# Optimization experiments

Measured on AMD Instinct MI355X. Metric: run time of the kernel, lower is better.

The kernel has to match this reference:

```python
import jax, jax.numpy as jnp
import numpy as np

S = 8192  # query length
T = 8192  # key/value length
D = 256   # head dim


def setup_inputs() -> dict:
    key = jax.random.key(0)
    kq, kk, kv = jax.random.split(key, 3)
    return {
        "query": jax.random.normal(kq, (S, D), dtype=jnp.float32),
        "key": jax.random.normal(kk, (T, D), dtype=jnp.float32),
        "value": jax.random.normal(kv, (T, D), dtype=jnp.float32),
    }


def reference(query, key, value):
    # attn_weights = Q @ K^T  (contract last dims, no batch dims)  -> [S, T]
    attn_weights = jnp.einsum("sd,td->st", query, key)
    # SoftmaxAttn: softmax over axes [ndim//2, ndim) == last axis for 2D
    attn_weights = jax.nn.softmax(attn_weights, axis=-1).astype(jnp.float32)
    # y = A @ V  -> [S, D]
    y = jnp.einsum("st,td->sd", attn_weights, value)
    return y
```

## Files before the change

### kernel.cpp

```cpp
#include <hip/hip_runtime.h>
#include <hip/hip_fp16.h>

#define S_LEN 8192
#define T_LEN 8192
#define D_DIM 256
#define QBLK 256
#define KVBLK 32
#define TSPLIT 8
#define TCHUNK (T_LEN / TSPLIT)
#define NKV (TCHUNK / KVBLK)
#define NQT (S_LEN / QBLK)
#define KTILE_BYTES 16384
#define VTILE_BYTES 16384
#define RESCALE_THR 4.0f

typedef _Float16 f16x8 __attribute__((ext_vector_type(8)));
typedef float f32x4 __attribute__((ext_vector_type(4)));

struct h4 { _Float16 h[4]; };

#define GLOAD_LDS16(g, l)                                              \
    __builtin_amdgcn_global_load_lds(                                  \
        (const __attribute__((address_space(1))) void*)(g),            \
        (__attribute__((address_space(3))) void*)(l), 16, 0, 0)

#define MFMA16(a, b, c) __builtin_amdgcn_mfma_f32_16x16x32_f16(a, b, c, 0, 0, 0)

__global__ __launch_bounds__(256) void cvt_kernel(const float* __restrict__ in,
                                                  _Float16* __restrict__ out, int n4) {
    int i = blockIdx.x * 256 + threadIdx.x;
    if (i < n4) {
        float4 v = ((const float4*)in)[i];
        h4 o;
        o.h[0] = (_Float16)v.x; o.h[1] = (_Float16)v.y;
        o.h[2] = (_Float16)v.z; o.h[3] = (_Float16)v.w;
        ((h4*)out)[i] = o;
    }
}

__global__ __launch_bounds__(256) void cvt_swz_kernel(const float* __restrict__ in,
                                                      _Float16* __restrict__ img,
                                                      int nchunks) {
    int id = blockIdx.x * 256 + threadIdx.x;
    if (id >= nchunks) return;
    int row = id >> 5, ck = id & 31;
    int t = row >> 5, r = row & 31;
    float4 a = *(const float4*)(in + (size_t)row * D_DIM + ck * 8);
    float4 b = *(const float4*)(in + (size_t)row * D_DIM + ck * 8 + 4);
    f16x8 o;
    o[0] = (_Float16)a.x; o[1] = (_Float16)a.y; o[2] = (_Float16)a.z; o[3] = (_Float16)a.w;
    o[4] = (_Float16)b.x; o[5] = (_Float16)b.y; o[6] = (_Float16)b.z; o[7] = (_Float16)b.w;
    *(f16x8*)((char*)img + (size_t)t * KTILE_BYTES + r * 512 + ((ck ^ (r & 7)) << 4)) = o;
}

__global__ __launch_bounds__(256) void vt_swz_kernel(const float* __restrict__ V,
                                                     _Float16* __restrict__ Vimg) {
    __shared__ float tile[32][260];
    const int t = blockIdx.x;
#pragma unroll
    for (int i = 0; i < 8; ++i) {
        int idx = i * 256 + threadIdx.x;
        int kr = idx >> 6, c4 = idx & 63;
        float4 v = *(const float4*)(V + ((size_t)t * 32 + kr) * D_DIM + c4 * 4);
        tile[kr][c4 * 4 + 0] = v.x;
        tile[kr][c4 * 4 + 1] = v.y;
        tile[kr][c4 * 4 + 2] = v.z;
        tile[kr][c4 * 4 + 3] = v.w;
    }
    __syncthreads();
#pragma unroll
    for (int i = 0; i < 4; ++i) {
        int gid = i * 256 + threadIdx.x;
        int d = gid >> 2, gk = gid & 3;
        f16x8 o;
#pragma unroll
        for (int j = 0; j < 8; ++j) o[j] = (_Float16)tile[gk * 8 + j][d];
        *(f16x8*)((char*)Vimg + (size_t)t * VTILE_BYTES + d * 64 +
                  ((gk ^ (d & 3)) << 4)) = o;
    }
}

__global__ __launch_bounds__(512, 2) void attn_kernel(
    const _Float16* __restrict__ Qh, const _Float16* __restrict__ Kimg,
    const _Float16* __restrict__ Vimg, _Float16* __restrict__ Opart,
    float* __restrict__ ml) {
    __shared__ __align__(16) char smem[65536];
    const int tid = threadIdx.x;
    const int wave = tid >> 6, lane = tid & 63;
    const int g = lane >> 4, c = lane & 15;
    const int qtile = blockIdx.x, split = blockIdx.y;
    const int tile0 = split * NKV;

    f16x8 qf[2][8];
    {
        const size_t qrow0 = (size_t)qtile * QBLK + wave * 32 + c;
#pragma unroll
        for (int mi = 0; mi < 2; ++mi)
#pragma unroll
            for (int ks = 0; ks < 8; ++ks)
                qf[mi][ks] =
                    *(const f16x8*)(Qh + (qrow0 + mi * 16) * D_DIM + (ks * 4 + g) * 8);
    }

    f32x4 acc[2][16];
#pragma unroll
    for (int mi = 0; mi < 2; ++mi)
#pragma unroll
        for (int dt = 0; dt < 16; ++dt) acc[mi][dt] = (f32x4){0.f, 0.f, 0.f, 0.f};
    float m[2] = {-1e30f, -1e30f}, l[2] = {0.f, 0.f};

    const int stg_l = wave * 1024;
    const int stg_g = stg_l + lane * 16;

    {
        const char* Kt = (const char*)Kimg + (size_t)tile0 * KTILE_BYTES;
        const char* Vt = (const char*)Vimg + (size_t)tile0 * VTILE_BYTES;
#pragma unroll
        for (int i = 0; i < 2; ++i) {
            GLOAD_LDS16(Kt + i * 8192 + stg_g, smem + i * 8192 + stg_l);
            GLOAD_LDS16(Vt + i * 8192 + stg_g, smem + 32768 + i * 8192 + stg_l);
        }
    }

    for (int kt = 0; kt < NKV; ++kt) {
        const int cur = kt & 1;
        if (kt + 1 < NKV) {
            const char* Kt = (const char*)Kimg + (size_t)(tile0 + kt + 1) * KTILE_BYTES;
            const char* Vt = (const char*)Vimg + (size_t)(tile0 + kt + 1) * VTILE_BYTES;
            const int nb = (cur ^ 1) * 16384;
#pragma unroll
            for (int i = 0; i < 2; ++i) {
                GLOAD_LDS16(Kt + i * 8192 + stg_g, smem + nb + i * 8192 + stg_l);
                GLOAD_LDS16(Vt + i * 8192 + stg_g, smem + 32768 + nb + i * 8192 + stg_l);
            }
            asm volatile("s_waitcnt vmcnt(4)" ::: "memory");
        } else {
            asm volatile("s_waitcnt vmcnt(0)" ::: "memory");
        }
        __builtin_amdgcn_s_barrier();

        const char* sK = smem + cur * 16384;
        const char* sV = smem + 32768 + cur * 16384;

        f32x4 st[2][2];
#pragma unroll
        for (int mi = 0; mi < 2; ++mi)
#pragma unroll
            for (int ct = 0; ct < 2; ++ct) st[mi][ct] = (f32x4){0.f, 0.f, 0.f, 0.f};
        __builtin_amdgcn_s_setprio(1);
#pragma unroll
        for (int ks = 0; ks < 8; ++ks) {
            const int ck = ((ks * 4 + g) ^ (c & 7)) << 4;
            f16x8 kf0 = *(const f16x8*)(sK + c * 512 + ck);
            f16x8 kf1 = *(const f16x8*)(sK + 8192 + c * 512 + ck);
            st[0][0] = MFMA16(kf0, qf[0][ks], st[0][0]);
            st[0][1] = MFMA16(kf1, qf[0][ks], st[0][1]);
            st[1][0] = MFMA16(kf0, qf[1][ks], st[1][0]);
            st[1][1] = MFMA16(kf1, qf[1][ks], st[1][1]);
        }
        __builtin_amdgcn_s_setprio(0);

        unsigned int pk[2][2][2];
#pragma unroll
        for (int mi = 0; mi < 2; ++mi) {
            float pm = st[mi][0][0];
#pragma unroll
            for (int ct = 0; ct < 2; ++ct)
#pragma unroll
                for (int r = 0; r < 4; ++r) pm = fmaxf(pm, st[mi][ct][r]);
            pm = fmaxf(pm, __shfl_xor(pm, 16));
            pm = fmaxf(pm, __shfl_xor(pm, 32));
            if (__any(pm > m[mi] + RESCALE_THR)) {
                float mn = fmaxf(m[mi], pm);
                float sc = __expf(m[mi] - mn);
                m[mi] = mn;
                l[mi] *= sc;
                float fr[4];
#pragma unroll
                for (int r = 0; r < 4; ++r) fr[r] = __shfl(sc, (g << 4) | (g * 4 + r));
#pragma unroll
                for (int dt = 0; dt < 16; ++dt)
#pragma unroll
                    for (int r = 0; r < 4; ++r) acc[mi][dt][r] *= fr[r];
            }
            float rs = 0.f;
#pragma unroll
            for (int ct = 0; ct < 2; ++ct)
#pragma unroll
                for (int r = 0; r < 4; ++r) {
                    float p = __expf(st[mi][ct][r] - m[mi]);
                    st[mi][ct][r] = p;
                    rs += p;
                }
            rs += __shfl_xor(rs, 16);
            rs += __shfl_xor(rs, 32);
            l[mi] += rs;
#pragma unroll
            for (int ct = 0; ct < 2; ++ct) {
                pk[mi][ct][0] = __builtin_bit_cast(
                    unsigned int,
                    __builtin_amdgcn_cvt_pkrtz(st[mi][ct][0], st[mi][ct][1]));
                pk[mi][ct][1] = __builtin_bit_cast(
                    unsigned int,
                    __builtin_amdgcn_cvt_pkrtz(st[mi][ct][2], st[mi][ct][3]));
            }
        }

        union PU { unsigned int u[4]; f16x8 v; };
        PU pu[2];
#pragma unroll
        for (int mi = 0; mi < 2; ++mi)
#pragma unroll
            for (int w = 0; w < 4; ++w) {
                int src = ((((g & 1) << 1) + (w >> 1)) << 4) | c;
                int t0 = __shfl((int)pk[mi][0][w & 1], src);
                int t1 = __shfl((int)pk[mi][1][w & 1], src);
                pu[mi].u[w] = (unsigned int)((g >> 1) ? t1 : t0);
            }

        __builtin_amdgcn_s_setprio(1);
#pragma unroll
        for (int dt = 0; dt < 16; ++dt) {
            f16x8 vf = *(const f16x8*)(sV + (dt * 16 + c) * 64 + ((g ^ (c & 3)) << 4));
            acc[0][dt] = MFMA16(pu[0].v, vf, acc[0][dt]);
            acc[1][dt] = MFMA16(pu[1].v, vf, acc[1][dt]);
        }
        __builtin_amdgcn_s_setprio(0);

        __builtin_amdgcn_s_barrier();
    }

    _Float16* Ob = Opart + (size_t)(qtile * TSPLIT + split) * QBLK * D_DIM;
#pragma unroll
    for (int mi = 0; mi < 2; ++mi)
#pragma unroll
        for (int dt = 0; dt < 16; ++dt)
#pragma unroll
            for (int r = 0; r < 4; ++r) {
                int row = wave * 32 + mi * 16 + g * 4 + r;
                int col = dt * 16 + c;
                Ob[(size_t)row * D_DIM + col] = (_Float16)acc[mi][dt][r];
            }
    if (g == 0) {
        float* mlb = ml + (size_t)((qtile * TSPLIT + split) * QBLK) * 2;
#pragma unroll
        for (int mi = 0; mi < 2; ++mi) {
            int row = wave * 32 + mi * 16 + c;
            mlb[row * 2 + 0] = m[mi];
            mlb[row * 2 + 1] = l[mi];
        }
    }
}

__global__ __launch_bounds__(256) void combine_kernel(const _Float16* __restrict__ Opart,
                                                      const float* __restrict__ ml,
                                                      float* __restrict__ out) {
    int r = blockIdx.x;
    int qtile = r >> 8, rl = r & 255;
    int d = threadIdx.x;
    float mv[TSPLIT], lv[TSPLIT];
    float M = -1e30f;
#pragma unroll
    for (int s = 0; s < TSPLIT; ++s) {
        const float* mlb = ml + (size_t)((qtile * TSPLIT + s) * QBLK + rl) * 2;
        mv[s] = mlb[0];
        lv[s] = mlb[1];
        M = fmaxf(M, mv[s]);
    }
    float num = 0.f, den = 0.f;
#pragma unroll
    for (int s = 0; s < TSPLIT; ++s) {
        float w = __expf(mv[s] - M);
        num += w * (float)Opart[((size_t)(qtile * TSPLIT + s) * QBLK + rl) * D_DIM + d];
        den += w * lv[s];
    }
    out[(size_t)r * D_DIM + d] = num / den;
}

extern "C" void kernel_launch(void* const* d_in, const int* in_sizes, int n_in,
                              void* d_out, int out_size, void* d_ws, size_t ws_size,
                              hipStream_t stream) {
    const float* Q = (const float*)d_in[0];
    const float* K = (const float*)d_in[1];
    const float* V = (const float*)d_in[2];
    float* out = (float*)d_out;
    char* ws = (char*)d_ws;

    _Float16* Qh = (_Float16*)ws;
    _Float16* Kimg = (_Float16*)(ws + (4 << 20));
    _Float16* Vimg = (_Float16*)(ws + (8 << 20));
    _Float16* Opart = (_Float16*)(ws + (12 << 20));
    float* ml = (float*)(ws + (44 << 20));

    const int n4 = S_LEN * D_DIM / 4;
    const int nchunks = S_LEN * D_DIM / 8;
    cvt_kernel<<<n4 / 256, 256, 0, stream>>>(Q, Qh, n4);
    cvt_swz_kernel<<<nchunks / 256, 256, 0, stream>>>(K, Kimg, nchunks);
    vt_swz_kernel<<<T_LEN / 32, 256, 0, stream>>>(V, Vimg);
    dim3 ag(NQT, TSPLIT);
    attn_kernel<<<ag, 512, 0, stream>>>(Qh, Kimg, Vimg, Opart, ml);
    combine_kernel<<<S_LEN, 256, 0, stream>>>(Opart, ml, out);
}
```

Before: 115.2 us.

## Fold log2e into Q, permute V layout to drop P shuffles, halve Q block

Q is pre-scaled by log2(e) during conversion, so the softmax uses exp2f directly. The V image is rebuilt with a permuted key order and a new swizzle, so the packed P fragments from the QK MFMA output can feed the PV MFMA without cross-lane shuffles. The attention block shrinks to 256 threads with QBLK 128, which doubles the grid, and the staging loads and vmcnt waits are adjusted to match. The rescale threshold is raised, which adds fp16 overflow headroom risk in exchange for fewer rescales. Halving QBLK also halves K/V reuse per block.

```diff
diff --git a/kernel.cpp b/kernel.cpp
--- a/kernel.cpp
+++ b/kernel.cpp
@@ -4,7 +4,7 @@
 #define S_LEN 8192
 #define T_LEN 8192
 #define D_DIM 256
-#define QBLK 256
+#define QBLK 128
 #define KVBLK 32
 #define TSPLIT 8
 #define TCHUNK (T_LEN / TSPLIT)
@@ -12,7 +12,8 @@
 #define NQT (S_LEN / QBLK)
 #define KTILE_BYTES 16384
 #define VTILE_BYTES 16384
-#define RESCALE_THR 4.0f
+#define RESCALE_THR 6.0f
+#define LOG2E 1.44269504f
 
 typedef _Float16 f16x8 __attribute__((ext_vector_type(8)));
 typedef float f32x4 __attribute__((ext_vector_type(4)));
@@ -32,8 +33,8 @@
     if (i < n4) {
         float4 v = ((const float4*)in)[i];
         h4 o;
-        o.h[0] = (_Float16)v.x; o.h[1] = (_Float16)v.y;
-        o.h[2] = (_Float16)v.z; o.h[3] = (_Float16)v.w;
+        o.h[0] = (_Float16)(v.x * LOG2E); o.h[1] = (_Float16)(v.y * LOG2E);
+        o.h[2] = (_Float16)(v.z * LOG2E); o.h[3] = (_Float16)(v.w * LOG2E);
         ((h4*)out)[i] = o;
     }
 }
@@ -74,13 +75,14 @@
         int d = gid >> 2, gk = gid & 3;
         f16x8 o;
 #pragma unroll
-        for (int j = 0; j < 8; ++j) o[j] = (_Float16)tile[gk * 8 + j][d];
+        for (int j = 0; j < 8; ++j)
+            o[j] = (_Float16)tile[(j >> 2) * 16 + gk * 4 + (j & 3)][d];
         *(f16x8*)((char*)Vimg + (size_t)t * VTILE_BYTES + d * 64 +
-                  ((gk ^ (d & 3)) << 4)) = o;
-    }
-}
-
-__global__ __launch_bounds__(512, 2) void attn_kernel(
+                  ((gk ^ ((d >> 1) & 3)) << 4)) = o;
+    }
+}
+
+__global__ __launch_bounds__(256, 2) void attn_kernel(
     const _Float16* __restrict__ Qh, const _Float16* __restrict__ Kimg,
     const _Float16* __restrict__ Vimg, _Float16* __restrict__ Opart,
     float* __restrict__ ml) {
@@ -101,6 +103,7 @@
                 qf[mi][ks] =
                     *(const f16x8*)(Qh + (qrow0 + mi * 16) * D_DIM + (ks * 4 + g) * 8);
     }
+    asm volatile("s_waitcnt vmcnt(0)" ::: "memory");
 
     f32x4 acc[2][16];
 #pragma unroll
@@ -109,16 +112,15 @@
         for (int dt = 0; dt < 16; ++dt) acc[mi][dt] = (f32x4){0.f, 0.f, 0.f, 0.f};
     float m[2] = {-1e30f, -1e30f}, l[2] = {0.f, 0.f};
 
-    const int stg_l = wave * 1024;
-    const int stg_g = stg_l + lane * 16;
+    const int othr = tid * 16;
 
     {
         const char* Kt = (const char*)Kimg + (size_t)tile0 * KTILE_BYTES;
         const char* Vt = (const char*)Vimg + (size_t)tile0 * VTILE_BYTES;
 #pragma unroll
-        for (int i = 0; i < 2; ++i) {
-            GLOAD_LDS16(Kt + i * 8192 + stg_g, smem + i * 8192 + stg_l);
-            GLOAD_LDS16(Vt + i * 8192 + stg_g, smem + 32768 + i * 8192 + stg_l);
+        for (int i = 0; i < 4; ++i) {
+            GLOAD_LDS16(Kt + i * 4096 + othr, smem + i * 4096 + othr);
+            GLOAD_LDS16(Vt + i * 4096 + othr, smem + 32768 + i * 4096 + othr);
         }
     }
 
@@ -129,11 +131,11 @@
             const char* Vt = (const char*)Vimg + (size_t)(tile0 + kt + 1) * VTILE_BYTES;
             const int nb = (cur ^ 1) * 16384;
 #pragma unroll
-            for (int i = 0; i < 2; ++i) {
-                GLOAD_LDS16(Kt + i * 8192 + stg_g, smem + nb + i * 8192 + stg_l);
-                GLOAD_LDS16(Vt + i * 8192 + stg_g, smem + 32768 + nb + i * 8192 + stg_l);
+            for (int i = 0; i < 4; ++i) {
+                GLOAD_LDS16(Kt + i * 4096 + othr, smem + nb + i * 4096 + othr);
+                GLOAD_LDS16(Vt + i * 4096 + othr, smem + 32768 + nb + i * 4096 + othr);
             }
-            asm volatile("s_waitcnt vmcnt(4)" ::: "memory");
+            asm volatile("s_waitcnt vmcnt(8)" ::: "memory");
         } else {
             asm volatile("s_waitcnt vmcnt(0)" ::: "memory");
         }
@@ -160,7 +162,8 @@
         }
         __builtin_amdgcn_s_setprio(0);
 
-        unsigned int pk[2][2][2];
+        union PU { unsigned int u[4]; f16x8 v; };
+        PU pu[2];
 #pragma unroll
         for (int mi = 0; mi < 2; ++mi) {
             float pm = st[mi][0][0];
@@ -172,7 +175,7 @@
             pm = fmaxf(pm, __shfl_xor(pm, 32));
             if (__any(pm > m[mi] + RESCALE_THR)) {
                 float mn = fmaxf(m[mi], pm);
-                float sc = __expf(m[mi] - mn);
+                float sc = exp2f(m[mi] - mn);
                 m[mi] = mn;
                 l[mi] *= sc;
                 float fr[4];
@@ -188,40 +191,28 @@
             for (int ct = 0; ct < 2; ++ct)
 #pragma unroll
                 for (int r = 0; r < 4; ++r) {
-                    float p = __expf(st[mi][ct][r] - m[mi]);
+                    float p = exp2f(st[mi][ct][r] - m[mi]);
                     st[mi][ct][r] = p;
                     rs += p;
                 }
             rs += __shfl_xor(rs, 16);
             rs += __shfl_xor(rs, 32);
             l[mi] += rs;
-#pragma unroll
-            for (int ct = 0; ct < 2; ++ct) {
-                pk[mi][ct][0] = __builtin_bit_cast(
-                    unsigned int,
-                    __builtin_amdgcn_cvt_pkrtz(st[mi][ct][0], st[mi][ct][1]));
-                pk[mi][ct][1] = __builtin_bit_cast(
-                    unsigned int,
-                    __builtin_amdgcn_cvt_pkrtz(st[mi][ct][2], st[mi][ct][3]));
-            }
-        }
-
-        union PU { unsigned int u[4]; f16x8 v; };
-        PU pu[2];
-#pragma unroll
-        for (int mi = 0; mi < 2; ++mi)
-#pragma unroll
-            for (int w = 0; w < 4; ++w) {
-                int src = ((((g & 1) << 1) + (w >> 1)) << 4) | c;
-                int t0 = __shfl((int)pk[mi][0][w & 1], src);
-                int t1 = __shfl((int)pk[mi][1][w & 1], src);
-                pu[mi].u[w] = (unsigned int)((g >> 1) ? t1 : t0);
-            }
+            pu[mi].u[0] = __builtin_bit_cast(
+                unsigned int, __builtin_amdgcn_cvt_pkrtz(st[mi][0][0], st[mi][0][1]));
+            pu[mi].u[1] = __builtin_bit_cast(
+                unsigned int, __builtin_amdgcn_cvt_pkrtz(st[mi][0][2], st[mi][0][3]));
+            pu[mi].u[2] = __builtin_bit_cast(
+                unsigned int, __builtin_amdgcn_cvt_pkrtz(st[mi][1][0], st[mi][1][1]));
+            pu[mi].u[3] = __builtin_bit_cast(
+                unsigned int, __builtin_amdgcn_cvt_pkrtz(st[mi][1][2], st[mi][1][3]));
+        }
 
         __builtin_amdgcn_s_setprio(1);
 #pragma unroll
         for (int dt = 0; dt < 16; ++dt) {
-            f16x8 vf = *(const f16x8*)(sV + (dt * 16 + c) * 64 + ((g ^ (c & 3)) << 4));
+            const int d = dt * 16 + c;
+            f16x8 vf = *(const f16x8*)(sV + d * 64 + ((g ^ ((c >> 1) & 3)) << 4));
             acc[0][dt] = MFMA16(pu[0].v, vf, acc[0][dt]);
             acc[1][dt] = MFMA16(pu[1].v, vf, acc[1][dt]);
         }
@@ -256,7 +247,7 @@
                                                       const float* __restrict__ ml,
                                                       float* __restrict__ out) {
     int r = blockIdx.x;
-    int qtile = r >> 8, rl = r & 255;
+    int qtile = r >> 7, rl = r & 127;
     int d = threadIdx.x;
     float mv[TSPLIT], lv[TSPLIT];
     float M = -1e30f;
@@ -270,7 +261,7 @@
     float num = 0.f, den = 0.f;
 #pragma unroll
     for (int s = 0; s < TSPLIT; ++s) {
-        float w = __expf(mv[s] - M);
+        float w = exp2f(mv[s] - M);
         num += w * (float)Opart[((size_t)(qtile * TSPLIT + s) * QBLK + rl) * D_DIM + d];
         den += w * lv[s];
     }
@@ -298,6 +289,6 @@
     cvt_swz_kernel<<<nchunks / 256, 256, 0, stream>>>(K, Kimg, nchunks);
     vt_swz_kernel<<<T_LEN / 32, 256, 0, stream>>>(V, Vimg);
     dim3 ag(NQT, TSPLIT);
-    attn_kernel<<<ag, 512, 0, stream>>>(Qh, Kimg, Vimg, Opart, ml);
+    attn_kernel<<<ag, 256, 0, stream>>>(Qh, Kimg, Vimg, Opart, ml);
     combine_kernel<<<S_LEN, 256, 0, stream>>>(Opart, ml, out);
 }
```

After: 110.7 us. 3.9% less time.
